# Kernel tuning notes

Measured on AMD Instinct MI355X. Metric: run time of the kernel, lower is better.

Reference implementation:

```python
import jax, jax.numpy as jnp
import numpy as np
from jax.scipy.linalg import solve_triangular

KERN = 3
STRIDE = 2
EPS = 1e-6


def setup_inputs() -> dict:
    key = jax.random.key(0)
    k1, k2 = jax.random.split(key)
    B, C, H, W, n = 4, 8, 20, 20, 8
    O = 16
    # raw randn, then make each (n,n) slice SPD: A A^T / n + 0.5 I
    A = jax.random.normal(k1, (B, C, H, W, n, n), dtype=jnp.float32)
    x = A @ jnp.swapaxes(A, -1, -2) / n + 0.5 * jnp.eye(n, dtype=jnp.float32)
    weight_matrix = jax.random.uniform(k2, (O, KERN * KERN * C), dtype=jnp.float32)
    return {"x": x, "weight_matrix": weight_matrix}


def weight_normalize(w):
    # row-wise: w_i^2 / (sum_j w_j^2 + eps)  (vectorized form of the torch loop)
    w2 = w ** 2
    return w2 / (jnp.sum(w2, axis=-1, keepdims=True) + EPS)


def _extract_windows(x, k, s):
    # x: (B,C,H,W,n,n) -> (B,Ho,Wo, k*k*C, n, n) matching torch's
    # unfold/permute/view ordering: merged window index = (kh, kw, c)
    B, C, H, W, n, _ = x.shape
    Ho = (H - k) // s + 1
    Wo = (W - k) // s + 1
    i0 = (jnp.arange(Ho) * s)[:, None] + jnp.arange(k)  # (Ho,k)
    j0 = (jnp.arange(Wo) * s)[:, None] + jnp.arange(k)  # (Wo,k)
    xw = x[:, :, i0]            # (B,C,Ho,k,W,n,n)
    xw = xw[:, :, :, :, j0]     # (B,C,Ho,k,Wo,k,n,n)
    xw = xw.transpose(0, 2, 4, 3, 5, 1, 6, 7)  # (B,Ho,Wo,kh,kw,C,n,n)
    return xw.reshape(B, Ho, Wo, k * k * C, n, n), Ho, Wo


def _recursive_fm(mats, t):
    # Weighted recursive Frechet mean on the SPD manifold (affine-invariant
    # metric), as in ManifoldNet: M_k = geodesic(M_{k-1}, X_k; t_k).
    # Using G with G G^T = M (Cholesky), geodesic = G (G^{-1} X G^{-T})^t G^T.
    # Since t[0]==1, starting from identity reproduces M_1 = X_1 exactly.
    n = mats.shape[-1]

    def step(M, xt):
        X, tk = xt
        L = jnp.linalg.cholesky(M)
        Y = solve_triangular(L, X, lower=True)        # L^{-1} X
        Z = solve_triangular(L, Y.T, lower=True)      # L^{-1} X L^{-T}
        Z = 0.5 * (Z + Z.T)
        ev, V = jnp.linalg.eigh(Z)
        ev = jnp.clip(ev, 1e-10)
        Zt = (V * ev ** tk) @ V.T                      # Z^{tk}
        Mn = L @ Zt @ L.T
        return 0.5 * (Mn + Mn.T), None

    M, _ = jax.lax.scan(step, jnp.eye(n, dtype=mats.dtype), (mats, t))
    return M


def reference(x, weight_matrix):
    B, C, H, W, n, _ = x.shape
    xw, Ho, Wo = _extract_windows(x, KERN, STRIDE)   # (B,Ho,Wo,N,n,n)
    N = xw.shape[3]
    wn = weight_normalize(weight_matrix)             # (O,N), rows sum ~1
    t = wn / jnp.cumsum(wn, axis=-1)                 # t[:,0] == 1
    xflat = xw.reshape(-1, N, n, n)                  # (S,N,n,n), S=B*Ho*Wo
    fm_sites = jax.vmap(_recursive_fm, in_axes=(0, None))   # over sites
    fm_all = jax.vmap(fm_sites, in_axes=(None, 0))           # over out-channels
    out = fm_all(xflat, t)                           # (O,S,n,n)
    O = weight_matrix.shape[0]
    out = out.reshape(O, B, Ho, Wo, n, n).transpose(1, 0, 2, 3, 4, 5)
    return out  # (B,O,Ho,Wo,n,n); torch module returns (this, 0)
```

## Files before the change

### kernel.cpp

```cpp
#include <hip/hip_runtime.h>
#include <utility>


static __device__ __forceinline__ float bper(int byteidx, float v) {
  return __int_as_float(__builtin_amdgcn_ds_bpermute(byteidx, __float_as_int(v)));
}
static __device__ __forceinline__ float rl(float v, int lane_u) {
  return __int_as_float(__builtin_amdgcn_readlane(__float_as_int(v), lane_u));
}
template <int P>
static __device__ __forceinline__ float swz(float v) {
  return __int_as_float(__builtin_amdgcn_ds_swizzle(__float_as_int(v), P));
}
static __device__ __forceinline__ float dpp_ror8(float v) {
  return __int_as_float(__builtin_amdgcn_update_dpp(0, __float_as_int(v), 0x128, 0xF, 0xF, true));
}
static __device__ __forceinline__ float rcpf_(float x) { return __builtin_amdgcn_rcpf(x); }
static __device__ __forceinline__ float rsqf_(float x) { return __builtin_amdgcn_rsqf(x); }

template <int R>
static __device__ __forceinline__ float obcast(float v, bool hi) {
  const int x = __float_as_int(v);
  const int a = __builtin_amdgcn_update_dpp(0, x, (R & 3) * 0x55, 0xF, 0xF, false);
  const int m = __builtin_amdgcn_update_dpp(0, a, 0x141, 0xF, 0xF, false);
  const int r = (R < 4) ? (hi ? m : a) : (hi ? a : m);
  return __int_as_float(r);
}

template <class F, int... Is>
static __device__ __forceinline__ void sfor_impl(F&& f, std::integer_sequence<int, Is...>) {
  (f(std::integral_constant<int, Is>{}), ...);
}
template <int N, class F>
static __device__ __forceinline__ void sfor(F&& f) {
  sfor_impl(static_cast<F&&>(f), std::make_integer_sequence<int, N>{});
}

__global__ __launch_bounds__(64) void spd_fm_kernel(
    const float* __restrict__ x,
    const float* __restrict__ wm,
    float* __restrict__ out)
{
  const int wid = blockIdx.x;
  const int lane = threadIdx.x;
  const int i = lane >> 3, j = lane & 7;
  const bool hi = (lane & 4) != 0;

  const int o    = wid / 324;
  const int site = wid - o * 324;
  const int b   = site / 81;
  const int r81 = site - b * 81;
  const int ho  = r81 / 9;
  const int wo  = r81 - ho * 9;

  const float* xb   = x + b * 204800 + (ho * 2) * 1280 + (wo * 2) * 64 + lane;
  const float* wrow = wm + o * 72;

  const int tp      = (((j << 3) | i)) << 2;
  const int jj5     = j << 5;
  const int j2      = j << 2;
  const int bx_ii   = (i * 9) << 2;
  const int bx_self = lane << 2;

  float w0 = wrow[0];
  float csum = w0 * w0;
  float M = xb[0];
  M = 0.5f * (M + bper(tp, M));

  float Xc = xb[25600];
  for (int k = 1; k < 72; ++k) {
    float Xn = 0.0f;
    if (k + 1 < 72) {
      const int k1 = k + 1;
      const int kh = k1 / 24;
      const int rr = k1 - kh * 24;
      Xn = xb[(rr & 7) * 25600 + kh * 1280 + (rr >> 3) * 64];
    }

    float wv = wrow[k];
    wv *= wv;
    csum += wv;
    const float tk = wv * rcpf_(csum);

    float a = M;
    float dinv = 0.0f;
    sfor<8>([&](auto KK) {
      constexpr int kk = KK.value;
      const float akk  = fmaxf(rl(a, 9 * kk), 1e-20f);
      const float rinv = rsqf_(akk);
      if (j == kk) a = (i == kk) ? akk * rinv : a * rinv;
      if (i == kk && j == kk) dinv = rinv;
      const float lik = obcast<kk>(a, hi);
      const float ljk = bper(jj5 | (kk << 2), a);
      if (i > kk && j > kk) a = fmaf(-lik, ljk, a);
    });
    const float Lm = (j <= i) ? a : 0.0f;

    float lir[8];
    sfor<8>([&](auto RR) {
      constexpr int r = RR.value;
      lir[r] = swz<(r << 5) | 0x18>(Lm);
    });

    float y = Xc;
    sfor<8>([&](auto RR) {
      constexpr int r = RR.value;
      const float dr = rl(dinv, 9 * r);
      if (i == r) y *= dr;
      const float yr = bper((r << 5) | j2, y);
      if (i > r) y = fmaf(-lir[r], yr, y);
    });

    float z = bper(tp, y);
    sfor<8>([&](auto RR) {
      constexpr int r = RR.value;
      const float dr = rl(dinv, 9 * r);
      if (i == r) z *= dr;
      const float zr = bper((r << 5) | j2, z);
      if (i > r) z = fmaf(-lir[r], zr, z);
    });
    z = 0.5f * (z + bper(tp, z));

    float D = bper(bx_ii, z);
    float t8 = D + dpp_ror8(D);
    t8 += swz<0x401F>(t8);
    const float trz = t8 + bper(bx_self ^ 128, t8);
    const float s2 = 3.9e-7f * trz * trz;

    float W = bper(tp, Lm);
    auto jacobi_sweep = [&]() {
      sfor<7>([&](auto RR) {
        constexpr int r   = RR.value + 1;
        constexpr int xc  = r << 2;
        constexpr int xr  = r << 5;
        constexpr int msb = (r >= 4) ? 4 : ((r >= 2) ? 2 : 1);
        float zr, Dq, Wr;
        if constexpr (r < 4) {
          constexpr int P = ((r << 3) << 10) | 0x1F;
          zr = swz<P>(z);
          Dq = swz<P>(D);
          Wr = swz<P>(W);
        } else {
          zr = bper(bx_self ^ xr, z);
          Dq = bper(bx_self ^ xr, D);
          Wr = bper(bx_self ^ xr, W);
        }
        const float aR = bper(bx_ii ^ xc, z);
        const float dd = D - Dq;
        const float q2 = aR + aR;
        const float h2 = fmaf(dd, dd, q2 * q2);
        const float rh = rsqf_(fmaxf(h2, 1e-38f));
        const float c2 = fmaf(0.5f * fabsf(dd), rh, 0.5f);
        const float rc = rsqf_(c2);
        const bool ok  = h2 > 1e-38f;
        const float cc = ok ? c2 * rc : 1.0f;
        const float tt = aR * (rh * rc);
        const bool neg = (dd < 0.0f) || ((dd == 0.0f) && ((i & msb) != 0));
        float sR = neg ? -tt : tt;
        sR = ok ? sR : 0.0f;
        const float G = fmaf(sR, zr, cc * z);
        W = fmaf(sR, Wr, cc * W);
        D = fmaf(cc, fmaf(cc, D, sR * aR), sR * fmaf(cc, aR, sR * Dq));
        const float T  = bper(tp, G);
        const float T2 = bper(tp ^ xc, G);
        z = fmaf(sR, T2, cc * T);
      });
    };
    jacobi_sweep();
    jacobi_sweep();
#pragma unroll 1
    for (int s = 2; s < 5; ++s) {
      const bool off = (i < j) && (z * z > s2);
      if (__ballot(off) == 0ull) break;
      jacobi_sweep();
    }

    const float evd = (i == j) ? fmaxf(z, 1e-10f) : 1.0f;
    const float wd  = __builtin_amdgcn_exp2f(tk * __builtin_amdgcn_logf(evd));

    const float U = bper(tp, W);
    float mn = 0.0f;
    sfor<8>([&](auto KK) {
      constexpr int kk = KK.value;
      const float wk  = rl(wd, 9 * kk);
      const float uik = swz<(kk << 5) | 0x18>(U);
      const float ujk = bper(jj5 | (kk << 2), U);
      mn = fmaf(wk * uik, ujk, mn);
    });
    M = 0.5f * (mn + bper(tp, mn));
    Xc = Xn;
  }

  out[(size_t)((b * 16 + o) * 81 + r81) * 64 + lane] = M;
}

extern "C" void kernel_launch(void* const* d_in, const int* in_sizes, int n_in,
                              void* d_out, int out_size, void* d_ws, size_t ws_size,
                              hipStream_t stream) {
  const float* x  = (const float*)d_in[0];
  const float* wm = (const float*)d_in[1];
  float* out = (float*)d_out;
  spd_fm_kernel<<<5184, 64, 0, stream>>>(x, wm, out);
}
```

Baseline: 770.1 us.

## Restructure whitening via L^{-1} and drop extra triangular solve; loosen Jacobi stopping

New measurement: 784.4 us. No clear change (+1.9%).

```diff
diff --git a/kernel.cpp b/kernel.cpp
--- a/kernel.cpp
+++ b/kernel.cpp
@@ -103,29 +103,32 @@
     });
 
     float y = Xc;
+    float v = (i == j) ? 1.0f : 0.0f;
     sfor<8>([&](auto RR) {
       constexpr int r = RR.value;
       const float dr = rl(dinv, 9 * r);
-      if (i == r) y *= dr;
+      if (i == r) { y *= dr; v *= dr; }
       const float yr = bper((r << 5) | j2, y);
-      if (i > r) y = fmaf(-lir[r], yr, y);
-    });
-
-    float z = bper(tp, y);
-    sfor<8>([&](auto RR) {
-      constexpr int r = RR.value;
-      const float dr = rl(dinv, 9 * r);
-      if (i == r) z *= dr;
-      const float zr = bper((r << 5) | j2, z);
-      if (i > r) z = fmaf(-lir[r], zr, z);
-    });
-    z = 0.5f * (z + bper(tp, z));
+      const float vr = bper((r << 5) | j2, v);
+      if (i > r) {
+        y = fmaf(-lir[r], yr, y);
+        v = fmaf(-lir[r], vr, v);
+      }
+    });
+
+    float z = 0.0f;
+    sfor<8>([&](auto KK) {
+      constexpr int kk = KK.value;
+      const float lik = swz<(kk << 5) | 0x18>(v);
+      const float yjk = bper(jj5 | (kk << 2), y);
+      z = fmaf(lik, yjk, z);
+    });
 
     float D = bper(bx_ii, z);
     float t8 = D + dpp_ror8(D);
     t8 += swz<0x401F>(t8);
     const float trz = t8 + bper(bx_self ^ 128, t8);
-    const float s2 = 3.9e-7f * trz * trz;
+    const float s2 = 1.0e-6f * trz * trz;
 
     float W = bper(tp, Lm);
     auto jacobi_sweep = [&]() {
@@ -169,23 +172,23 @@
     jacobi_sweep();
     jacobi_sweep();
 #pragma unroll 1
-    for (int s = 2; s < 5; ++s) {
+    for (int s = 2; s < 4; ++s) {
       const bool off = (i < j) && (z * z > s2);
       if (__ballot(off) == 0ull) break;
       jacobi_sweep();
     }
 
-    const float evd = (i == j) ? fmaxf(z, 1e-10f) : 1.0f;
-    const float wd  = __builtin_amdgcn_exp2f(tk * __builtin_amdgcn_logf(evd));
-
-    const float U = bper(tp, W);
+    const float wdl = __builtin_amdgcn_exp2f(tk * __builtin_amdgcn_logf(fmaxf(D, 1e-10f)));
+    const float wdT = bper(tp, wdl);
+
+    const float U   = bper(tp, W);
+    const float Usc = U * wdT;
     float mn = 0.0f;
     sfor<8>([&](auto KK) {
       constexpr int kk = KK.value;
-      const float wk  = rl(wd, 9 * kk);
-      const float uik = swz<(kk << 5) | 0x18>(U);
-      const float ujk = bper(jj5 | (kk << 2), U);
-      mn = fmaf(wk * uik, ujk, mn);
+      const float a1 = swz<(kk << 5) | 0x18>(Usc);
+      const float a2 = bper(jj5 | (kk << 2), U);
+      mn = fmaf(a1, a2, mn);
     });
     M = 0.5f * (mn + bper(tp, mn));
     Xc = Xn;
```
